# Performance work log

Hardware: AMD Instinct MI355X
Metric: run time of the kernel (lower is better)

The kernel has to match this reference:

```python
import jax, jax.numpy as jnp
import numpy as np

B, T, D_IN, D_OUT = 16, 2048, 2048, 2048
N_ADAPTERS, RANK = 8, 16


def setup_inputs() -> dict:
    key = jax.random.key(0)
    k_x, k_w, k_a, k_b, k_s, k_idx = jax.random.split(key, 6)
    x = jax.random.normal(k_x, (B, T, D_IN), dtype=jnp.float32)
    # frozen base weight (nn.Linear stores W as (d_out, d_in)); bias=False
    W = jax.random.normal(k_w, (D_OUT, D_IN), dtype=jnp.float32) * (1.0 / np.sqrt(D_IN))
    # stacked adapter bank: A[a] is (r, d_in), Bm[a] is (d_out, r)
    A = jax.random.normal(k_a, (N_ADAPTERS, RANK, D_IN), dtype=jnp.float32) * 0.02
    Bm = jax.random.normal(k_b, (N_ADAPTERS, D_OUT, RANK), dtype=jnp.float32) * 0.02
    scalings = jnp.ones((N_ADAPTERS,), dtype=jnp.float32)  # alpha / r, pre-merged
    adapter_idx = jax.random.randint(k_idx, (B,), 0, N_ADAPTERS, dtype=jnp.int32)
    return {"x": x, "W": W, "A": A, "Bm": Bm, "scalings": scalings,
            "adapter_idx": adapter_idx}


def reference(x, W, A, Bm, scalings, adapter_idx):
    # base path: H = x @ W^T   -> (B, T, d_out)
    H = jnp.einsum("btd,od->bto", x, W)
    # per-request adapter gather (replaces the Python loop over adapter groups)
    A_b = A[adapter_idx]          # (B, r, d_in)
    B_b = Bm[adapter_idx]         # (B, d_out, r)
    s_b = scalings[adapter_idx]   # (B,)
    # low-rank delta: (x @ A^T) @ B^T, done per request, fully batched
    xa = jnp.einsum("btd,brd->btr", x, A_b)        # (B, T, r)
    delta = jnp.einsum("btr,bor->bto", xa, B_b)    # (B, T, d_out)
    # original computes delta under torch.no_grad() with detached A/B
    delta = jax.lax.stop_gradient(delta * s_b[:, None, None])
    return H + delta
```

## Files before the change

### kernel.cpp

```cpp
#include <hip/hip_runtime.h>
#include <stdint.h>

typedef unsigned short u16;
typedef __attribute__((ext_vector_type(4))) short s16x4;
typedef __attribute__((ext_vector_type(8))) short short8;
typedef __attribute__((ext_vector_type(4))) float f32x4;

static __device__ __forceinline__ u16 f2bf(float f) {
    union { float f; uint32_t u; } c; c.f = f;
    uint32_t u = c.u;
    u += 0x7FFFu + ((u >> 16) & 1u);
    return (u16)(u >> 16);
}

#define D_IN   2048
#define D_OUT  2048
#define MTOT   32768
#define BK     64
#define NTM    32

__device__ __forceinline__ void gload16(const u16* g, u16* l) {
    __builtin_amdgcn_global_load_lds(
        (const __attribute__((address_space(1))) void*)g,
        (__attribute__((address_space(3))) void*)l, 16, 0, 0);
}

__global__ __launch_bounds__(256) void k_prep(
    const float* __restrict__ W, const float* __restrict__ A, const float* __restrict__ Bm,
    u16* __restrict__ Wb, u16* __restrict__ Ap, u16* __restrict__ Bp)
{
    const int b = blockIdx.x, tid = threadIdx.x;
    if (b < 2048) {
        int i = (b * 256 + tid) * 8;
        const float4* p = (const float4*)(W + i);
        float4 v0 = p[0], v1 = p[1];
        short8 o;
        o[0]=f2bf(v0.x); o[1]=f2bf(v0.y); o[2]=f2bf(v0.z); o[3]=f2bf(v0.w);
        o[4]=f2bf(v1.x); o[5]=f2bf(v1.y); o[6]=f2bf(v1.z); o[7]=f2bf(v1.w);
        *(short8*)(Wb + i) = o;
    } else if (b < 6144) {
        int i = (b - 2048) * 256 + tid;
        int d = i & 2047, r = (i >> 11) & 63, a = i >> 17;
        Ap[i] = (r < 16) ? f2bf(A[(((a << 4) + r) << 11) + d]) : (u16)0;
    } else {
        int i = (b - 6144) * 256 + tid;
        int j = i & 63, n = (i >> 6) & 2047, a = i >> 17;
        Bp[i] = (j < 16) ? f2bf(Bm[((((a << 11) + n)) << 4) + j]) : (u16)0;
    }
}

__global__ __launch_bounds__(256) void k_cast_x_xa(
    const float* __restrict__ x, const u16* __restrict__ Ap,
    const float* __restrict__ scal, const int* __restrict__ aidx,
    u16* __restrict__ xb, u16* __restrict__ xa)
{
    __shared__ __align__(16) u16 Xs[32 * BK];
    __shared__ __align__(16) u16 Ps[64 * BK];
    const int tid = threadIdx.x, lane = tid & 63, wid = tid >> 6;
    const int m0 = blockIdx.x << 5;
    const int a = aidx[m0 >> 11];
    const float s = scal[a];
    const int wr = wid >> 1, wc = wid & 1;
    const int arow = (wr << 4) + (lane & 15);
    const int brow = (wc << 5) + (lane & 15);
    const int scol = ((lane & 7) ^ (lane >> 3)) << 3;

    f32x4 acc[2];
    acc[0] = 0.f; acc[1] = 0.f;

    const int xrow_l = tid >> 4;
    const int xcol   = (tid & 15) << 2;
    const int wslot  = (tid & 15) >> 1;
    const int wsub   = (tid & 1) << 2;

    const u16* apg = Ap + ((size_t)a << 17);
    const u16* gP[2]; u16* lP[2];
    #pragma unroll
    for (int it = 0; it < 2; ++it) {
        const int chunk = (wid << 1) + it;
        const int row = (chunk << 3) + (lane >> 3);
        gP[it] = apg + ((size_t)row << 11) + scol;
        lP[it] = Ps + (chunk << 9) + (lane << 3);
    }

    for (int kt = 0; kt < NTM; ++kt) {
        const int k0 = kt << 6;
        float4 xv[2];
        #pragma unroll
        for (int j = 0; j < 2; ++j)
            xv[j] = *(const float4*)(x + ((size_t)(m0 + (j << 4) + xrow_l) << 11) + k0 + xcol);
        #pragma unroll
        for (int j = 0; j < 2; ++j) {
            const int row = (j << 4) + xrow_l;
            s16x4 c4;
            c4[0]=f2bf(xv[j].x); c4[1]=f2bf(xv[j].y); c4[2]=f2bf(xv[j].z); c4[3]=f2bf(xv[j].w);
            *(s16x4*)(Xs + (row << 6) + ((wslot ^ (row & 7)) << 3) + wsub) = c4;
            *(s16x4*)(xb + ((size_t)(m0 + row) << 11) + k0 + xcol) = c4;
        }
        gload16(gP[0] + k0, lP[0]);
        gload16(gP[1] + k0, lP[1]);
        asm volatile("s_waitcnt vmcnt(0)" ::: "memory");
        __syncthreads();
        #pragma unroll
        for (int kk = 0; kk < 2; ++kk) {
            const int sl = ((kk << 2) + (lane >> 4)) ^ (lane & 7);
            short8 af = *(const short8*)(Xs + (arow << 6) + (sl << 3));
            #pragma unroll
            for (int ni = 0; ni < 2; ++ni) {
                short8 bv = *(const short8*)(Ps + ((brow + ni * 16) << 6) + (sl << 3));
                acc[ni] = __builtin_amdgcn_mfma_f32_16x16x32_bf16(af, bv, acc[ni], 0, 0, 0);
            }
        }
        __syncthreads();
    }

    #pragma unroll
    for (int ni = 0; ni < 2; ++ni) {
        const int cc = (wc << 5) + ni * 16 + (lane & 15);
        #pragma unroll
        for (int rr = 0; rr < 4; ++rr) {
            const int mm = m0 + (wr << 4) + ((lane >> 4) << 2) + rr;
            xa[((size_t)mm << 6) + cc] = f2bf(acc[ni][rr] * s);
        }
    }
}

__global__ __launch_bounds__(512, 2) void k_gemm(
    const u16* __restrict__ xb, const u16* __restrict__ Wb,
    const u16* __restrict__ xa, const u16* __restrict__ Bp,
    const int* __restrict__ aidx, float* __restrict__ out)
{
    __shared__ __align__(16) u16 LDS[2 * 32768];
    const int tid = threadIdx.x, lane = tid & 63, wid = tid >> 6;

    const int newbid = (blockIdx.x & 7) * 128 + (blockIdx.x >> 3);
    const int bm = newbid >> 3, bn = newbid & 7;
    const int m0 = bm << 8, n0 = bn << 8;
    const int wr = wid >> 2, wc = wid & 3;
    const int a = aidx[m0 >> 11];

    f32x4 acc[8][4];
    #pragma unroll
    for (int i = 0; i < 8; ++i)
        #pragma unroll
        for (int j = 0; j < 4; ++j) acc[i][j] = 0.0f;

    const int sc = ((tid & 7) ^ ((tid >> 3) & 7)) << 3;
    const int srw = tid >> 3;

    const int sl0 = (((lane >> 4)    ) ^ (lane & 7)) << 3;
    const int sl1 = (((lane >> 4) + 4) ^ (lane & 7)) << 3;
    const int aRowBase = (wr << 7) + (lane & 15);
    const int bRowBase = (wc << 6) + (lane & 15);

    short8 af[4][2], bv[4][2];

    auto STG = [&](const u16* ptr, int stride, int rowbase, int kofs, int ldsofs) {
        const u16* s_ = ptr + ((size_t)(rowbase + srw)) * stride + kofs + sc;
        gload16(s_,                          &LDS[ldsofs + (tid << 3)]);
        gload16(s_ + ((size_t)stride << 6),  &LDS[ldsofs + 4096 + (tid << 3)]);
    };
    auto SA = [&](int tt, int h) {
        const int lo = ((tt & 1) << 15) + (h << 13);
        if (tt < NTM) STG(xb, 2048, m0 + (h << 7), tt << 6, lo);
        else          STG(xa, 64,   m0 + (h << 7), 0,       lo);
    };
    auto SB = [&](int tt, int h) {
        const int lo = ((tt & 1) << 15) + 16384 + (h << 13);
        if (tt < NTM) STG(Wb, 2048, n0 + (h << 7), tt << 6, lo);
        else          STG(Bp, 64,   (a << 11) + n0 + (h << 7), 0, lo);
    };

    #define BAR  __builtin_amdgcn_s_barrier()
    #define LGK0 do { asm volatile("s_waitcnt lgkmcnt(0)" ::: "memory"); \
                      __builtin_amdgcn_sched_barrier(0); } while (0)

    #define RDA(c_, mq_) do { _Pragma("unroll")                                     \
        for (int mi = 0; mi < 4; ++mi) {                                            \
            const int row = aRowBase + ((mq_) << 6) + (mi << 4);                    \
            af[mi][0] = *(const short8*)&LDS[((c_) << 15) + (row << 6) + sl0];      \
            af[mi][1] = *(const short8*)&LDS[((c_) << 15) + (row << 6) + sl1];      \
        } } while (0)

    #define RDB(c_, ni_) do {                                                       \
            const int row = bRowBase + ((ni_) << 4);                                \
            bv[ni_][0] = *(const short8*)&LDS[((c_) << 15) + 16384 + (row << 6) + sl0]; \
            bv[ni_][1] = *(const short8*)&LDS[((c_) << 15) + 16384 + (row << 6) + sl1]; \
        } while (0)

    #define MM(mq_, ns_) do { __builtin_amdgcn_s_setprio(1); _Pragma("unroll")      \
        for (int kk = 0; kk < 2; ++kk) _Pragma("unroll")                            \
        for (int mi = 0; mi < 4; ++mi) _Pragma("unroll")                            \
        for (int j = 0; j < 2; ++j)                                                 \
            acc[(mq_) * 4 + mi][(ns_) * 2 + j] =                                    \
                __builtin_amdgcn_mfma_f32_16x16x32_bf16(af[mi][kk],                 \
                    bv[(ns_) * 2 + j][kk], acc[(mq_) * 4 + mi][(ns_) * 2 + j], 0, 0, 0); \
        __builtin_amdgcn_s_setprio(0); } while (0)

    SA(0, 0); SA(0, 1); SB(0, 0); SB(0, 1); SB(1, 0); SB(1, 1);
    asm volatile("s_waitcnt vmcnt(4)" ::: "memory");
    BAR;

    for (int t = 0; t <= NTM; ++t) {
        const int c = t & 1;
        RDB(c, 0); RDB(c, 1); RDA(c, 0);
        if (t + 1 <= NTM) SA(t + 1, 0);
        BAR; LGK0; MM(0, 0); BAR;
        RDB(c, 2); RDB(c, 3);
        if (t + 1 <= NTM) SA(t + 1, 1);
        BAR; LGK0; MM(0, 1); BAR;
        RDA(c, 1);
        if (t + 2 <= NTM) SB(t + 2, 0);
        BAR; LGK0; MM(1, 0); BAR;
        if (t + 2 <= NTM) SB(t + 2, 1);
        BAR; MM(1, 1);
        if (t < NTM - 1)      asm volatile("s_waitcnt vmcnt(4)" ::: "memory");
        else if (t == NTM - 1) asm volatile("s_waitcnt vmcnt(0)" ::: "memory");
        BAR;
    }

    #undef MM
    #undef RDB
    #undef RDA
    #undef LGK0
    #undef BAR

    #pragma unroll
    for (int mi = 0; mi < 8; ++mi) {
        #pragma unroll
        for (int ni = 0; ni < 4; ++ni) {
            const int nn = n0 + (wc << 6) + ni * 16 + (lane & 15);
            #pragma unroll
            for (int r = 0; r < 4; ++r) {
                const int mm = m0 + (wr << 7) + mi * 16 + ((lane >> 4) << 2) + r;
                out[((size_t)mm << 11) + nn] = acc[mi][ni][r];
            }
        }
    }
}

extern "C" void kernel_launch(void* const* d_in, const int* in_sizes, int n_in,
                              void* d_out, int out_size, void* d_ws, size_t ws_size,
                              hipStream_t stream) {
    const float* x  = (const float*)d_in[0];
    const float* W  = (const float*)d_in[1];
    const float* A  = (const float*)d_in[2];
    const float* Bm = (const float*)d_in[3];
    const float* sc = (const float*)d_in[4];
    const int* aidx = (const int*)d_in[5];
    float* out = (float*)d_out;

    char* ws = (char*)d_ws;
    u16* xb = (u16*)(ws);
    u16* Wb = (u16*)(ws + 134217728);
    u16* Ap = (u16*)(ws + 134217728 + 8388608);
    u16* Bp = (u16*)(ws + 134217728 + 8388608 + 2097152);
    u16* xa = (u16*)(ws + 134217728 + 8388608 + 2097152 + 2097152);

    hipLaunchKernelGGL(k_prep,      dim3(10240), dim3(256), 0, stream, W, A, Bm, Wb, Ap, Bp);
    hipLaunchKernelGGL(k_cast_x_xa, dim3(1024),  dim3(256), 0, stream, x, Ap, sc, aidx, xb, xa);
    hipLaunchKernelGGL(k_gemm,      dim3(1024),  dim3(512), 0, stream, xb, Wb, xa, Bp, aidx, out);
}
```

Before: 380.7 us.

## Merge prep and x-cast kernels, convert adapter A inline instead of precasting

Folds the W/Bm bf16 conversion into the same launch as the x-cast/xa kernel by giving extra blocks that work, removing one kernel launch and its serialization. The A-adapter bf16 padded copy is dropped. Each x-tile block now loads its 16 fp32 A rows directly, converts them and writes them into the swizzled LDS tile, with the padded rows zeroed once. This removes a global round trip for Ap and a launch boundary, at the cost of register-path loads replacing the async LDS DMA and repeated A reads per block.

```diff
diff --git a/kernel.cpp b/kernel.cpp
--- a/kernel.cpp
+++ b/kernel.cpp
@@ -25,63 +25,60 @@
         (__attribute__((address_space(3))) void*)l, 16, 0, 0);
 }
 
-__global__ __launch_bounds__(256) void k_prep(
-    const float* __restrict__ W, const float* __restrict__ A, const float* __restrict__ Bm,
-    u16* __restrict__ Wb, u16* __restrict__ Ap, u16* __restrict__ Bp)
-{
-    const int b = blockIdx.x, tid = threadIdx.x;
-    if (b < 2048) {
-        int i = (b * 256 + tid) * 8;
-        const float4* p = (const float4*)(W + i);
-        float4 v0 = p[0], v1 = p[1];
-        short8 o;
-        o[0]=f2bf(v0.x); o[1]=f2bf(v0.y); o[2]=f2bf(v0.z); o[3]=f2bf(v0.w);
-        o[4]=f2bf(v1.x); o[5]=f2bf(v1.y); o[6]=f2bf(v1.z); o[7]=f2bf(v1.w);
-        *(short8*)(Wb + i) = o;
-    } else if (b < 6144) {
-        int i = (b - 2048) * 256 + tid;
-        int d = i & 2047, r = (i >> 11) & 63, a = i >> 17;
-        Ap[i] = (r < 16) ? f2bf(A[(((a << 4) + r) << 11) + d]) : (u16)0;
-    } else {
-        int i = (b - 6144) * 256 + tid;
-        int j = i & 63, n = (i >> 6) & 2047, a = i >> 17;
-        Bp[i] = (j < 16) ? f2bf(Bm[((((a << 11) + n)) << 4) + j]) : (u16)0;
-    }
-}
-
-__global__ __launch_bounds__(256) void k_cast_x_xa(
-    const float* __restrict__ x, const u16* __restrict__ Ap,
+__global__ __launch_bounds__(256) void k_pre(
+    const float* __restrict__ x, const float* __restrict__ W,
+    const float* __restrict__ A, const float* __restrict__ Bm,
     const float* __restrict__ scal, const int* __restrict__ aidx,
-    u16* __restrict__ xb, u16* __restrict__ xa)
+    u16* __restrict__ xb, u16* __restrict__ Wb, u16* __restrict__ Bp,
+    u16* __restrict__ xa)
 {
     __shared__ __align__(16) u16 Xs[32 * BK];
     __shared__ __align__(16) u16 Ps[64 * BK];
-    const int tid = threadIdx.x, lane = tid & 63, wid = tid >> 6;
-    const int m0 = blockIdx.x << 5;
+    const int b = blockIdx.x, tid = threadIdx.x;
+
+    if (b >= 1024) {
+        if (b < 3072) {
+            int i = ((b - 1024) * 256 + tid) * 8;
+            const float4* p = (const float4*)(W + i);
+            float4 v0 = p[0], v1 = p[1];
+            short8 o;
+            o[0]=f2bf(v0.x); o[1]=f2bf(v0.y); o[2]=f2bf(v0.z); o[3]=f2bf(v0.w);
+            o[4]=f2bf(v1.x); o[5]=f2bf(v1.y); o[6]=f2bf(v1.z); o[7]=f2bf(v1.w);
+            *(short8*)(Wb + i) = o;
+        } else {
+            int i = (b - 3072) * 256 + tid;
+            int j = i & 63, n = (i >> 6) & 2047, a = i >> 17;
+            Bp[i] = (j < 16) ? f2bf(Bm[((((a << 11) + n)) << 4) + j]) : (u16)0;
+        }
+        return;
+    }
+
+    const int lane = tid & 63, wid = tid >> 6;
+    const int m0 = b << 5;
     const int a = aidx[m0 >> 11];
     const float s = scal[a];
     const int wr = wid >> 1, wc = wid & 1;
     const int arow = (wr << 4) + (lane & 15);
     const int brow = (wc << 5) + (lane & 15);
-    const int scol = ((lane & 7) ^ (lane >> 3)) << 3;
 
     f32x4 acc[2];
     acc[0] = 0.f; acc[1] = 0.f;
+
+    {
+        s16x4 z; z[0]=0; z[1]=0; z[2]=0; z[3]=0;
+        #pragma unroll
+        for (int j = 0; j < 3; ++j)
+            *(s16x4*)(Ps + 1024 + tid * 12 + j * 4) = z;
+    }
 
     const int xrow_l = tid >> 4;
     const int xcol   = (tid & 15) << 2;
     const int wslot  = (tid & 15) >> 1;
     const int wsub   = (tid & 1) << 2;
-
-    const u16* apg = Ap + ((size_t)a << 17);
-    const u16* gP[2]; u16* lP[2];
-    #pragma unroll
-    for (int it = 0; it < 2; ++it) {
-        const int chunk = (wid << 1) + it;
-        const int row = (chunk << 3) + (lane >> 3);
-        gP[it] = apg + ((size_t)row << 11) + scol;
-        lP[it] = Ps + (chunk << 9) + (lane << 3);
-    }
+    const int prow  = tid >> 4;
+    const int pcolg = tid & 15;
+    const float* Arow = A + ((size_t)((a << 4) + prow) << 11) + (pcolg << 2);
+    u16* pdst = Ps + (prow << 6) + ((((pcolg >> 1) ^ (prow & 7))) << 3) + ((pcolg & 1) << 2);
 
     for (int kt = 0; kt < NTM; ++kt) {
         const int k0 = kt << 6;
@@ -89,6 +86,7 @@
         #pragma unroll
         for (int j = 0; j < 2; ++j)
             xv[j] = *(const float4*)(x + ((size_t)(m0 + (j << 4) + xrow_l) << 11) + k0 + xcol);
+        float4 av = *(const float4*)(Arow + k0);
         #pragma unroll
         for (int j = 0; j < 2; ++j) {
             const int row = (j << 4) + xrow_l;
@@ -97,9 +95,11 @@
             *(s16x4*)(Xs + (row << 6) + ((wslot ^ (row & 7)) << 3) + wsub) = c4;
             *(s16x4*)(xb + ((size_t)(m0 + row) << 11) + k0 + xcol) = c4;
         }
-        gload16(gP[0] + k0, lP[0]);
-        gload16(gP[1] + k0, lP[1]);
-        asm volatile("s_waitcnt vmcnt(0)" ::: "memory");
+        {
+            s16x4 a4;
+            a4[0]=f2bf(av.x); a4[1]=f2bf(av.y); a4[2]=f2bf(av.z); a4[3]=f2bf(av.w);
+            *(s16x4*)pdst = a4;
+        }
         __syncthreads();
         #pragma unroll
         for (int kk = 0; kk < 2; ++kk) {
@@ -253,11 +253,11 @@
     char* ws = (char*)d_ws;
     u16* xb = (u16*)(ws);
     u16* Wb = (u16*)(ws + 134217728);
-    u16* Ap = (u16*)(ws + 134217728 + 8388608);
     u16* Bp = (u16*)(ws + 134217728 + 8388608 + 2097152);
     u16* xa = (u16*)(ws + 134217728 + 8388608 + 2097152 + 2097152);
 
-    hipLaunchKernelGGL(k_prep,      dim3(10240), dim3(256), 0, stream, W, A, Bm, Wb, Ap, Bp);
-    hipLaunchKernelGGL(k_cast_x_xa, dim3(1024),  dim3(256), 0, stream, x, Ap, sc, aidx, xb, xa);
-    hipLaunchKernelGGL(k_gemm,      dim3(1024),  dim3(512), 0, stream, xb, Wb, xa, Bp, aidx, out);
-}
+    hipLaunchKernelGGL(k_pre,  dim3(7168), dim3(256), 0, stream,
+                       x, W, A, Bm, sc, aidx, xb, Wb, Bp, xa);
+    hipLaunchKernelGGL(k_gemm, dim3(1024), dim3(512), 0, stream,
+                       xb, Wb, xa, Bp, aidx, out);
+}
```

Result: faster. 369.7 us, median of 2 (-2.9%).
